# Performance work log

Measured on AMD Instinct MI355X. Metric: run time of the kernel, lower is better.

## Reference

```python
import jax, jax.numpy as jnp
import numpy as np

N = 65536
D_IN = 784
H = 20
D_OUT = 10
N_MID = 28  # fc2..fc29, all Linear(20,20)


def setup_inputs() -> dict:
    key = jax.random.key(0)
    ks = jax.random.split(key, 8)
    # PyTorch Linear default init: U(-1/sqrt(fan_in), 1/sqrt(fan_in)); uniform is fine for a reference.
    def uni(k, shape, fan_in):
        bound = 1.0 / np.sqrt(fan_in)
        return jax.random.uniform(k, shape, jnp.float32, -bound, bound)
    x = jax.random.normal(ks[0], (N, D_IN), jnp.float32)
    W1 = uni(ks[1], (H, D_IN), D_IN)
    b1 = uni(ks[2], (H,), D_IN)
    Wmid = uni(ks[3], (N_MID, H, H), H)   # stacked fc2..fc29 weights
    bmid = uni(ks[4], (N_MID, H), H)
    W30 = uni(ks[5], (D_OUT, H), H)
    b30 = uni(ks[6], (D_OUT,), H)
    return {"x": x, "W1": W1, "b1": b1, "Wmid": Wmid, "bmid": bmid, "W30": W30, "b30": b30}


def reference(x, W1, b1, Wmid, bmid, W30, b30):
    # fc1 + relu
    h = jax.nn.relu(x @ W1.T + b1)  # [N, 20]
    # fc2..fc29 + relu, identical structure -> scan over stacked params
    def step(h, wb):
        W, b = wb
        return jax.nn.relu(h @ W.T + b), None
    h, _ = jax.lax.scan(step, h, (Wmid, bmid))
    # fc30 (no relu)
    return h @ W30.T + b30  # [N, 10]
```

## Files before the change

### kernel.cpp

```cpp
#include <hip/hip_runtime.h>

typedef __attribute__((ext_vector_type(8))) short short8;
typedef __attribute__((ext_vector_type(16))) float f32x16;

#define MFMA(A, B, C) __builtin_amdgcn_mfma_f32_32x32x16_bf16(A, B, C, 0, 0, 0)

__device__ __forceinline__ float4 ldf4(const float* p) { return *(const float4*)p; }

__device__ __forceinline__ short8 mk8(unsigned w0, unsigned w1, unsigned w2, unsigned w3) {
    union { unsigned u[4]; short8 s; } t;
    t.u[0] = w0; t.u[1] = w1; t.u[2] = w2; t.u[3] = w3;
    return t.s;
}

__device__ __forceinline__ unsigned packhi2(float a, float b) {
    return __builtin_amdgcn_perm(__float_as_uint(b), __float_as_uint(a), 0x07060302u);
}
__device__ __forceinline__ float lopart(float v) {
    return v - __uint_as_float(__float_as_uint(v) & 0xFFFF0000u);
}

struct Frag { short8 h, l; };

__device__ __forceinline__ Frag cvt8(float4 a, float4 b) {
    Frag f;
    f.h = mk8(packhi2(a.x, a.y), packhi2(a.z, a.w),
              packhi2(b.x, b.y), packhi2(b.z, b.w));
    f.l = mk8(packhi2(lopart(a.x), lopart(a.y)), packhi2(lopart(a.z), lopart(a.w)),
              packhi2(lopart(b.x), lopart(b.y)), packhi2(lopart(b.z), lopart(b.w)));
    return f;
}

__device__ __forceinline__ void plswap(unsigned& lo, unsigned& hi) {
    asm("v_permlane32_swap_b32 %0, %1" : "+v"(lo), "+v"(hi));
}

__global__ __launch_bounds__(256, 2)
void mlp_mfma(const float* __restrict__ x,
              const float* __restrict__ W1, const float* __restrict__ b1,
              const float* __restrict__ Wmid, const float* __restrict__ bmid,
              const float* __restrict__ W30, const float* __restrict__ b30,
              float* __restrict__ out, int nrows)
{
    const int lane  = threadIdx.x & 63;
    const int wv    = threadIdx.x >> 6;
    const int tile  = blockIdx.x * 4 + wv;
    const int r0    = tile * 32;
    if (r0 >= nrows) return;
    const int colr  = lane & 31;
    const int half  = lane >> 5;
    const int row   = r0 + colr;

    f32x16 acc0, acc1;
#pragma unroll
    for (int r = 0; r < 16; ++r) { acc0[r] = 0.f; acc1[r] = 0.f; }

    const int   ow1  = colr < 20 ? colr : 19;
    const float* xr  = x  + (size_t)row * 784 + half * 8;
    const float* w1r = W1 + (size_t)ow1 * 784 + half * 8;

#pragma unroll 2
    for (int s = 0; s < 49; ++s) {
        const float4 xa = ldf4(xr + s * 16), xb = ldf4(xr + s * 16 + 4);
        const float4 wa = ldf4(w1r + s * 16), wb = ldf4(w1r + s * 16 + 4);
        Frag B = cvt8(xa, xb);
        Frag A = cvt8(wa, wb);
        if (s & 1) {
            acc1 = MFMA(A.h, B.h, acc1);
            acc1 = MFMA(A.l, B.h, acc1);
            acc1 = MFMA(A.h, B.l, acc1);
        } else {
            acc0 = MFMA(A.h, B.h, acc0);
            acc0 = MFMA(A.l, B.h, acc0);
            acc0 = MFMA(A.h, B.l, acc0);
        }
    }

    float Hv[16];
#pragma unroll
    for (int r = 0; r < 16; ++r) {
        const int o = (r & 3) + 8 * (r >> 2) + 4 * half;
        const float bv = b1[o < 20 ? o : 0];
        const float v  = fmaxf(acc0[r] + acc1[r] + bv, 0.f);
        Hv[r] = (o < 20) ? v : 0.f;
    }

    const int owm = colr < 20 ? colr : 19;
    const int ow3 = colr < 10 ? colr : 9;

#pragma unroll 1
    for (int l = 0; l < 29; ++l) {
        const bool last = (l == 28);
        const float* wrow = last ? (W30 + (size_t)ow3 * 20)
                                 : (Wmid + (size_t)l * 400 + (size_t)owm * 20);
        const float* bl   = last ? b30 : (bmid + l * 20);
        const int    omax = last ? 10 : 20;

        const float4 wa = ldf4(wrow + half * 8), wb = ldf4(wrow + half * 8 + 4);
        Frag A0 = cvt8(wa, wb);
        float4 wc = make_float4(0.f, 0.f, 0.f, 0.f);
        if (!half) wc = ldf4(wrow + 16);
        const short8 A1h = mk8(half ? 0u : packhi2(wc.x, wc.y),
                               half ? 0u : packhi2(wc.z, wc.w), 0u, 0u);
        const short8 A1l = mk8(half ? 0u : packhi2(lopart(wc.x), lopart(wc.y)),
                               half ? 0u : packhi2(lopart(wc.z), lopart(wc.w)), 0u, 0u);

        unsigned plo0 = packhi2(Hv[0], Hv[1]);
        unsigned plo1 = packhi2(Hv[2], Hv[3]);
        unsigned phi0 = packhi2(Hv[4], Hv[5]);
        unsigned phi1 = packhi2(Hv[6], Hv[7]);
        plswap(plo0, phi0);
        plswap(plo1, phi1);
        const short8 B0h = mk8(plo0, plo1, phi0, phi1);

        unsigned qlo0 = packhi2(lopart(Hv[0]), lopart(Hv[1]));
        unsigned qlo1 = packhi2(lopart(Hv[2]), lopart(Hv[3]));
        unsigned qhi0 = packhi2(lopart(Hv[4]), lopart(Hv[5]));
        unsigned qhi1 = packhi2(lopart(Hv[6]), lopart(Hv[7]));
        plswap(qlo0, qhi0);
        plswap(qlo1, qhi1);
        const short8 B0l = mk8(qlo0, qlo1, qhi0, qhi1);

        const short8 B1h = mk8(half ? 0u : packhi2(Hv[8], Hv[9]),
                               half ? 0u : packhi2(Hv[10], Hv[11]), 0u, 0u);
        const short8 B1l = mk8(half ? 0u : packhi2(lopart(Hv[8]), lopart(Hv[9])),
                               half ? 0u : packhi2(lopart(Hv[10]), lopart(Hv[11])), 0u, 0u);

        f32x16 acc;
#pragma unroll
        for (int r = 0; r < 16; ++r) {
            const int o = (r & 3) + 8 * (r >> 2) + 4 * half;
            const float bv = bl[o < omax ? o : 0];
            acc[r] = (o < omax) ? bv : 0.f;
        }
        acc = MFMA(A0.h, B0h, acc);
        acc = MFMA(A0.l, B0h, acc);
        acc = MFMA(A0.h, B0l, acc);
        acc = MFMA(A1h, B1h, acc);
        acc = MFMA(A1l, B1h, acc);
        acc = MFMA(A1h, B1l, acc);

        if (!last) {
#pragma unroll
            for (int r = 0; r < 16; ++r) {
                const int o = (r & 3) + 8 * (r >> 2) + 4 * half;
                Hv[r] = (o < 20) ? fmaxf(acc[r], 0.f) : 0.f;
            }
        } else {
#pragma unroll
            for (int r = 0; r < 16; ++r) {
                const int o = (r & 3) + 8 * (r >> 2) + 4 * half;
                if (o < 10) out[(size_t)row * 10 + o] = acc[r];
            }
        }
    }
}

extern "C" void kernel_launch(void* const* d_in, const int* in_sizes, int n_in,
                              void* d_out, int out_size, void* d_ws, size_t ws_size,
                              hipStream_t stream)
{
    const float* x    = (const float*)d_in[0];
    const float* W1   = (const float*)d_in[1];
    const float* b1   = (const float*)d_in[2];
    const float* Wmid = (const float*)d_in[3];
    const float* bmid = (const float*)d_in[4];
    const float* W30  = (const float*)d_in[5];
    const float* b30  = (const float*)d_in[6];
    float* out = (float*)d_out;

    const int nrows = in_sizes[0] / 784;
    const int tiles = (nrows + 31) / 32;
    const int grid  = (tiles + 3) / 4;
    mlp_mfma<<<grid, 256, 0, stream>>>(x, W1, b1, Wmid, bmid, W30, b30, out, nrows);
}
```

Measured before the change: 61.74 us.

## Prepack weights to bf16, split fc1 K across waves, fold bias into MFMA

Adds a prepack kernel that converts W1 to bf16 in MFMA fragment order and stores the mid/last layers as hi/lo bf16 fragments, with the bias placed in an extra K column so it is applied by the MFMA through a constant-one input. The fc1 layer drops the hi/lo split and uses a single bf16 MFMA per step, which lowers precision for the large 784-wide dot product. The fc1 K dimension is split across two waves per tile with an LDS reduction, and loads are software-pipelined. Occupancy hint goes from 2 to 4 blocks. The intent is to remove per-element conversion and triple-MFMA cost in the memory-bound fc1 stage, at the cost of an extra kernel launch and reduced accuracy.

```diff
diff --git a/kernel.cpp b/kernel.cpp
--- a/kernel.cpp
+++ b/kernel.cpp
@@ -2,155 +2,195 @@
 
 typedef __attribute__((ext_vector_type(8))) short short8;
 typedef __attribute__((ext_vector_type(16))) float f32x16;
+typedef unsigned short ushort16_t;
 
 #define MFMA(A, B, C) __builtin_amdgcn_mfma_f32_32x32x16_bf16(A, B, C, 0, 0, 0)
 
 __device__ __forceinline__ float4 ldf4(const float* p) { return *(const float4*)p; }
+__device__ __forceinline__ short8 ld8(const void* p) { return *(const short8*)p; }
 
 __device__ __forceinline__ short8 mk8(unsigned w0, unsigned w1, unsigned w2, unsigned w3) {
     union { unsigned u[4]; short8 s; } t;
     t.u[0] = w0; t.u[1] = w1; t.u[2] = w2; t.u[3] = w3;
     return t.s;
 }
-
 __device__ __forceinline__ unsigned packhi2(float a, float b) {
     return __builtin_amdgcn_perm(__float_as_uint(b), __float_as_uint(a), 0x07060302u);
 }
 __device__ __forceinline__ float lopart(float v) {
     return v - __uint_as_float(__float_as_uint(v) & 0xFFFF0000u);
 }
-
-struct Frag { short8 h, l; };
-
-__device__ __forceinline__ Frag cvt8(float4 a, float4 b) {
-    Frag f;
-    f.h = mk8(packhi2(a.x, a.y), packhi2(a.z, a.w),
-              packhi2(b.x, b.y), packhi2(b.z, b.w));
-    f.l = mk8(packhi2(lopart(a.x), lopart(a.y)), packhi2(lopart(a.z), lopart(a.w)),
-              packhi2(lopart(b.x), lopart(b.y)), packhi2(lopart(b.z), lopart(b.w)));
-    return f;
-}
-
 __device__ __forceinline__ void plswap(unsigned& lo, unsigned& hi) {
     asm("v_permlane32_swap_b32 %0, %1" : "+v"(lo), "+v"(hi));
 }
 
-__global__ __launch_bounds__(256, 2)
-void mlp_mfma(const float* __restrict__ x,
-              const float* __restrict__ W1, const float* __restrict__ b1,
-              const float* __restrict__ Wmid, const float* __restrict__ bmid,
-              const float* __restrict__ W30, const float* __restrict__ b30,
+__device__ __forceinline__ ushort16_t h16(float x) { return (ushort16_t)(__float_as_uint(x) >> 16); }
+__device__ __forceinline__ float fh(ushort16_t u) { return __uint_as_float(((unsigned)u) << 16); }
+
+__global__ void prepack(const float* __restrict__ W1,
+                        const float* __restrict__ Wmid, const float* __restrict__ bmid,
+                        const float* __restrict__ W30, const float* __restrict__ b30,
+                        ushort16_t* __restrict__ w1t, ushort16_t* __restrict__ midt)
+{
+    const int tid = blockIdx.x * 256 + threadIdx.x;
+    const int nth = gridDim.x * 256;
+    for (int i = tid; i < 49 * 512; i += nth) {
+        const int j = i & 7, hf = (i >> 3) & 1, o = (i >> 4) & 31, s = i >> 9;
+        const float v = (o < 20) ? W1[o * 784 + s * 16 + hf * 8 + j] : 0.f;
+        w1t[i] = h16(v);
+    }
+    for (int e = tid; e < 29 * 64; e += nth) {
+        const int hf = e & 1, o = (e >> 1) & 31, l = e >> 6;
+        ushort16_t v[32];
+#pragma unroll
+        for (int i = 0; i < 32; ++i) v[i] = 0;
+        const bool lastl = (l == 28);
+        const int omax = lastl ? 10 : 20;
+        if (o < omax) {
+            const float* wr = lastl ? (W30 + o * 20) : (Wmid + l * 400 + o * 20);
+            const float bias = lastl ? b30[o] : bmid[l * 20 + o];
+#pragma unroll
+            for (int j = 0; j < 8; ++j) {
+                const float w = wr[hf * 8 + j];
+                v[j]      = h16(w);
+                v[16 + j] = h16(w - fh(h16(w)));
+            }
+            if (hf == 0) {
+#pragma unroll
+                for (int j = 0; j < 4; ++j) {
+                    const float w = wr[16 + j];
+                    v[8 + j]  = h16(w);
+                    v[24 + j] = h16(w - fh(h16(w)));
+                }
+                v[12] = h16(bias);
+                v[13] = h16(bias - fh(h16(bias)));
+            }
+        }
+#pragma unroll
+        for (int i = 0; i < 32; ++i) midt[e * 32 + i] = v[i];
+    }
+}
+
+__global__ __launch_bounds__(256, 4)
+void mlp_main(const float* __restrict__ x, const float* __restrict__ b1p,
+              const ushort16_t* __restrict__ w1t, const ushort16_t* __restrict__ midt,
               float* __restrict__ out, int nrows)
 {
-    const int lane  = threadIdx.x & 63;
-    const int wv    = threadIdx.x >> 6;
-    const int tile  = blockIdx.x * 4 + wv;
-    const int r0    = tile * 32;
+    __shared__ float red[2][16][64];
+
+    const int lane = threadIdx.x & 63;
+    const int wv   = threadIdx.x >> 6;
+    const int kw   = wv & 1;
+    const int tl   = wv >> 1;
+    const int tile = blockIdx.x * 2 + tl;
+    const int r0   = tile * 32;
     if (r0 >= nrows) return;
-    const int colr  = lane & 31;
-    const int half  = lane >> 5;
-    const int row   = r0 + colr;
-
-    f32x16 acc0, acc1;
-#pragma unroll
-    for (int r = 0; r < 16; ++r) { acc0[r] = 0.f; acc1[r] = 0.f; }
-
-    const int   ow1  = colr < 20 ? colr : 19;
-    const float* xr  = x  + (size_t)row * 784 + half * 8;
-    const float* w1r = W1 + (size_t)ow1 * 784 + half * 8;
-
-#pragma unroll 2
-    for (int s = 0; s < 49; ++s) {
-        const float4 xa = ldf4(xr + s * 16), xb = ldf4(xr + s * 16 + 4);
-        const float4 wa = ldf4(w1r + s * 16), wb = ldf4(w1r + s * 16 + 4);
-        Frag B = cvt8(xa, xb);
-        Frag A = cvt8(wa, wb);
-        if (s & 1) {
-            acc1 = MFMA(A.h, B.h, acc1);
-            acc1 = MFMA(A.l, B.h, acc1);
-            acc1 = MFMA(A.h, B.l, acc1);
-        } else {
-            acc0 = MFMA(A.h, B.h, acc0);
-            acc0 = MFMA(A.l, B.h, acc0);
-            acc0 = MFMA(A.h, B.l, acc0);
+    const int colr = lane & 31;
+    const int half = lane >> 5;
+    const int row  = r0 + colr;
+
+    const int sbeg = kw ? 25 : 0;
+    const float* xp = x + (size_t)row * 784 + half * 8 + sbeg * 16;
+    const ushort16_t* at = w1t + sbeg * 512 + colr * 16 + half * 8;
+
+    f32x16 acc;
+#pragma unroll
+    for (int r = 0; r < 16; ++r) acc[r] = 0.f;
+
+    float4 a0 = ldf4(xp),      a1 = ldf4(xp + 4);
+    float4 a2 = ldf4(xp + 16), a3 = ldf4(xp + 20);
+    short8 Aa0 = ld8(at), Aa1 = ld8(at + 512);
+
+#pragma unroll 1
+    for (int cc = 0; cc < 6; ++cc) {
+        const float* q = xp + (2 * cc + 1) * 32;
+        const float4 c0 = ldf4(q),      c1 = ldf4(q + 4);
+        const float4 c2 = ldf4(q + 16), c3 = ldf4(q + 20);
+        const short8 Ab0 = ld8(at + (2 * cc + 1) * 1024);
+        const short8 Ab1 = ld8(at + (2 * cc + 1) * 1024 + 512);
+        acc = MFMA(Aa0, mk8(packhi2(a0.x, a0.y), packhi2(a0.z, a0.w),
+                            packhi2(a1.x, a1.y), packhi2(a1.z, a1.w)), acc);
+        acc = MFMA(Aa1, mk8(packhi2(a2.x, a2.y), packhi2(a2.z, a2.w),
+                            packhi2(a3.x, a3.y), packhi2(a3.z, a3.w)), acc);
+        if (cc < 5) {
+            const float* q2 = xp + (2 * cc + 2) * 32;
+            a0 = ldf4(q2);      a1 = ldf4(q2 + 4);
+            a2 = ldf4(q2 + 16); a3 = ldf4(q2 + 20);
+            Aa0 = ld8(at + (2 * cc + 2) * 1024);
+            Aa1 = ld8(at + (2 * cc + 2) * 1024 + 512);
         }
-    }
+        acc = MFMA(Ab0, mk8(packhi2(c0.x, c0.y), packhi2(c0.z, c0.w),
+                            packhi2(c1.x, c1.y), packhi2(c1.z, c1.w)), acc);
+        acc = MFMA(Ab1, mk8(packhi2(c2.x, c2.y), packhi2(c2.z, c2.w),
+                            packhi2(c3.x, c3.y), packhi2(c3.z, c3.w)), acc);
+    }
+    if (!kw) {
+        const float4 t0 = ldf4(xp + 384), t1 = ldf4(xp + 388);
+        const short8 At = ld8(at + 24 * 512);
+        acc = MFMA(At, mk8(packhi2(t0.x, t0.y), packhi2(t0.z, t0.w),
+                           packhi2(t1.x, t1.y), packhi2(t1.z, t1.w)), acc);
+    }
+
+    if (kw) {
+#pragma unroll
+        for (int r = 0; r < 16; ++r) red[tl][r][lane] = acc[r];
+    }
+    __syncthreads();
+    if (kw) return;
+#pragma unroll
+    for (int r = 0; r < 16; ++r) acc[r] += red[tl][r][lane];
 
     float Hv[16];
 #pragma unroll
     for (int r = 0; r < 16; ++r) {
         const int o = (r & 3) + 8 * (r >> 2) + 4 * half;
-        const float bv = b1[o < 20 ? o : 0];
-        const float v  = fmaxf(acc0[r] + acc1[r] + bv, 0.f);
-        Hv[r] = (o < 20) ? v : 0.f;
-    }
-
-    const int owm = colr < 20 ? colr : 19;
-    const int ow3 = colr < 10 ? colr : 9;
-
+        Hv[r] = fmaxf(acc[r] + b1p[o < 20 ? o : 0], 0.f);
+    }
+
+    const char* ap = (const char*)midt + (size_t)(colr * 2 + half) * 64;
 #pragma unroll 1
     for (int l = 0; l < 29; ++l) {
-        const bool last = (l == 28);
-        const float* wrow = last ? (W30 + (size_t)ow3 * 20)
-                                 : (Wmid + (size_t)l * 400 + (size_t)owm * 20);
-        const float* bl   = last ? b30 : (bmid + l * 20);
-        const int    omax = last ? 10 : 20;
-
-        const float4 wa = ldf4(wrow + half * 8), wb = ldf4(wrow + half * 8 + 4);
-        Frag A0 = cvt8(wa, wb);
-        float4 wc = make_float4(0.f, 0.f, 0.f, 0.f);
-        if (!half) wc = ldf4(wrow + 16);
-        const short8 A1h = mk8(half ? 0u : packhi2(wc.x, wc.y),
-                               half ? 0u : packhi2(wc.z, wc.w), 0u, 0u);
-        const short8 A1l = mk8(half ? 0u : packhi2(lopart(wc.x), lopart(wc.y)),
-                               half ? 0u : packhi2(lopart(wc.z), lopart(wc.w)), 0u, 0u);
-
-        unsigned plo0 = packhi2(Hv[0], Hv[1]);
-        unsigned plo1 = packhi2(Hv[2], Hv[3]);
-        unsigned phi0 = packhi2(Hv[4], Hv[5]);
-        unsigned phi1 = packhi2(Hv[6], Hv[7]);
-        plswap(plo0, phi0);
-        plswap(plo1, phi1);
+        const short8 A0h = ld8(ap), A1h = ld8(ap + 16);
+        const short8 A0l = ld8(ap + 32), A1l = ld8(ap + 48);
+        ap += 4096;
+
+        unsigned plo0 = packhi2(Hv[0], Hv[1]), plo1 = packhi2(Hv[2], Hv[3]);
+        unsigned phi0 = packhi2(Hv[4], Hv[5]), phi1 = packhi2(Hv[6], Hv[7]);
+        plswap(plo0, phi0); plswap(plo1, phi1);
         const short8 B0h = mk8(plo0, plo1, phi0, phi1);
 
         unsigned qlo0 = packhi2(lopart(Hv[0]), lopart(Hv[1]));
         unsigned qlo1 = packhi2(lopart(Hv[2]), lopart(Hv[3]));
         unsigned qhi0 = packhi2(lopart(Hv[4]), lopart(Hv[5]));
         unsigned qhi1 = packhi2(lopart(Hv[6]), lopart(Hv[7]));
-        plswap(qlo0, qhi0);
-        plswap(qlo1, qhi1);
+        plswap(qlo0, qhi0); plswap(qlo1, qhi1);
         const short8 B0l = mk8(qlo0, qlo1, qhi0, qhi1);
 
         const short8 B1h = mk8(half ? 0u : packhi2(Hv[8], Hv[9]),
-                               half ? 0u : packhi2(Hv[10], Hv[11]), 0u, 0u);
+                               half ? 0u : packhi2(Hv[10], Hv[11]),
+                               half ? 0u : 0x00003F80u, 0u);
         const short8 B1l = mk8(half ? 0u : packhi2(lopart(Hv[8]), lopart(Hv[9])),
-                               half ? 0u : packhi2(lopart(Hv[10]), lopart(Hv[11])), 0u, 0u);
-
-        f32x16 acc;
-#pragma unroll
-        for (int r = 0; r < 16; ++r) {
-            const int o = (r & 3) + 8 * (r >> 2) + 4 * half;
-            const float bv = bl[o < omax ? o : 0];
-            acc[r] = (o < omax) ? bv : 0.f;
-        }
-        acc = MFMA(A0.h, B0h, acc);
-        acc = MFMA(A0.l, B0h, acc);
-        acc = MFMA(A0.h, B0l, acc);
-        acc = MFMA(A1h, B1h, acc);
-        acc = MFMA(A1l, B1h, acc);
-        acc = MFMA(A1h, B1l, acc);
-
-        if (!last) {
+                               half ? 0u : packhi2(lopart(Hv[10]), lopart(Hv[11])),
+                               half ? 0u : 0x3F800000u, 0u);
+
+        f32x16 d;
+#pragma unroll
+        for (int r = 0; r < 16; ++r) d[r] = 0.f;
+        d = MFMA(A0h, B0h, d);
+        d = MFMA(A0l, B0h, d);
+        d = MFMA(A0h, B0l, d);
+        d = MFMA(A1h, B1h, d);
+        d = MFMA(A1l, B1h, d);
+        d = MFMA(A1h, B1l, d);
+
+        if (l < 28) {
+#pragma unroll
+            for (int r = 0; r < 16; ++r) Hv[r] = fmaxf(d[r], 0.f);
+        } else {
 #pragma unroll
             for (int r = 0; r < 16; ++r) {
                 const int o = (r & 3) + 8 * (r >> 2) + 4 * half;
-                Hv[r] = (o < 20) ? fmaxf(acc[r], 0.f) : 0.f;
-            }
-        } else {
-#pragma unroll
-            for (int r = 0; r < 16; ++r) {
-                const int o = (r & 3) + 8 * (r >> 2) + 4 * half;
-                if (o < 10) out[(size_t)row * 10 + o] = acc[r];
+                if (o < 10) out[(size_t)row * 10 + o] = d[r];
             }
         }
     }
@@ -169,8 +209,12 @@
     const float* b30  = (const float*)d_in[6];
     float* out = (float*)d_out;
 
+    ushort16_t* w1t  = (ushort16_t*)d_ws;
+    ushort16_t* midt = (ushort16_t*)((char*)d_ws + 50176);
+
     const int nrows = in_sizes[0] / 784;
+    prepack<<<32, 256, 0, stream>>>(W1, Wmid, bmid, W30, b30, w1t, midt);
     const int tiles = (nrows + 31) / 32;
-    const int grid  = (tiles + 3) / 4;
-    mlp_mfma<<<grid, 256, 0, stream>>>(x, W1, b1, Wmid, bmid, W30, b30, out, nrows);
-}
+    const int grid  = (tiles + 1) / 2;
+    mlp_main<<<grid, 256, 0, stream>>>(x, b1, w1t, midt, out, nrows);
+}
```

New measurement: 61.77 us. Within noise of the previous version (+0.1%).
